# Optimization experiments

Hardware: AMD Instinct MI355X
Metric: run time of the kernel (lower is better)

## Reference

```python
import jax, jax.numpy as jnp
import numpy as np

N = 50000      # nodes
E = 800000     # edges (avg degree 16)
IN = 512       # input features
OUT = 32       # per-head hidden features
H = 8          # heads (layer 1)
C = 16         # classes (layer 2, 1 head)
NEG_SLOPE = 0.2


def setup_inputs() -> dict:
    key = jax.random.key(0)
    ks = jax.random.split(key, 8)
    x = jax.random.normal(ks[0], (N, IN), jnp.float32)
    edge_index = jax.random.randint(ks[1], (2, E), 0, N, jnp.int32)
    # layer 1 params: W1 [IN, H*OUT], attention vectors a1_src/a1_dst [H, OUT]
    W1 = jax.random.normal(ks[2], (IN, H * OUT), jnp.float32) * (1.0 / np.sqrt(IN))
    a1_src = jax.random.normal(ks[3], (H, OUT), jnp.float32) * (1.0 / np.sqrt(OUT))
    a1_dst = jax.random.normal(ks[4], (H, OUT), jnp.float32) * (1.0 / np.sqrt(OUT))
    # layer 2 params: single head, W2 [H*OUT, C], a2_src/a2_dst [1, C]
    W2 = jax.random.normal(ks[5], (H * OUT, C), jnp.float32) * (1.0 / np.sqrt(H * OUT))
    a2_src = jax.random.normal(ks[6], (1, C), jnp.float32) * (1.0 / np.sqrt(C))
    a2_dst = jax.random.normal(ks[7], (1, C), jnp.float32) * (1.0 / np.sqrt(C))
    return {"x": x, "W1": W1, "a1_src": a1_src, "a1_dst": a1_dst,
            "W2": W2, "a2_src": a2_src, "a2_dst": a2_dst,
            "edge_index": edge_index}


def gat_layer(x, edge_index, W, a_src, a_dst, concat):
    """Standard GAT layer: e_ij = LeakyReLU(a_src.Wh_i + a_dst.Wh_j),
    softmax over incoming edges of each target node, scatter-aggregate."""
    n = x.shape[0]
    h_heads, f = a_src.shape
    h = (x @ W).reshape(n, h_heads, f)                      # [N, H, F]
    src, dst = edge_index[0], edge_index[1]
    es = jnp.einsum('nhf,hf->nh', h, a_src)                 # [N, H] per-node src scores
    ed = jnp.einsum('nhf,hf->nh', h, a_dst)                 # [N, H]
    e = jax.nn.leaky_relu(es[src] + ed[dst], NEG_SLOPE)     # [E, H] per-edge logits
    # segment softmax over edges grouped by dst node
    m = jax.ops.segment_max(e, dst, num_segments=n)         # [N, H]
    m = jnp.where(jnp.isfinite(m), m, 0.0)                  # empty segments -> -inf
    p = jnp.exp(e - m[dst])                                 # [E, H]
    s = jax.ops.segment_sum(p, dst, num_segments=n)         # [N, H]
    denom = s[dst]
    alpha = p / jnp.where(denom > 0, denom, 1.0)            # [E, H]
    msg = h[src] * alpha[:, :, None]                        # [E, H, F]
    out = jax.ops.segment_sum(msg, dst, num_segments=n)     # [N, H, F]
    if concat:
        return out.reshape(n, h_heads * f)
    return out.mean(axis=1)


def reference(x, W1, a1_src, a1_dst, W2, a2_src, a2_dst, edge_index):
    # dropout is identity in eval mode
    h = gat_layer(x, edge_index, W1, a1_src, a1_dst, concat=True)   # [N, H*OUT]
    h = jax.nn.elu(h)
    h = gat_layer(h, edge_index, W2, a2_src, a2_dst, concat=False)  # [N, C]
    return jax.nn.log_softmax(h, axis=1)
```

## Files before the change

### kernel.cpp

```cpp
#include <hip/hip_runtime.h>

#define NN 50000
#define EE 800000
#define KIN 512
#define HF 256
#define NH 8
#define FOUT 32
#define NC 16
#define NEG 0.2f
#define NB_SCAN 196
#define NP 50048

typedef unsigned short u16;
typedef __attribute__((ext_vector_type(8))) short shortx8;
typedef __attribute__((ext_vector_type(4))) float floatx4;
typedef __attribute__((ext_vector_type(8))) unsigned short ushortx8;
typedef __attribute__((ext_vector_type(4))) unsigned uintx4;

__device__ __forceinline__ float lrelu(float x) { return x > 0.f ? x : NEG * x; }

__device__ __forceinline__ u16 f2bf(float f) {
    unsigned u = __float_as_uint(f);
    return (u16)((u + 0x7FFFu + ((u >> 16) & 1u)) >> 16);
}
__device__ __forceinline__ float bf2f(u16 v) {
    return __uint_as_float((unsigned)v << 16);
}
__device__ __forceinline__ unsigned pk2bf(float a, float b) {
    unsigned ua = __float_as_uint(a), ub = __float_as_uint(b);
    return ((ua + 0x8000u) >> 16) | ((ub + 0x8000u) & 0xffff0000u);
}

__device__ __forceinline__ void gll16(const void* g, void* l) {
    __builtin_amdgcn_global_load_lds((const __attribute__((address_space(1))) void*)g,
                                     (__attribute__((address_space(3))) void*)l, 16, 0, 0);
}

__global__ void count_deg_convw(const int* __restrict__ dst, int* __restrict__ deg,
                                const float* __restrict__ x, const float* __restrict__ W1,
                                const float* __restrict__ W2,
                                u16* __restrict__ xb2, u16* __restrict__ w1t2,
                                u16* __restrict__ w2t) {
    int e = blockIdx.x * 256 + threadIdx.x;
    if (e < EE) {
        atomicAdd(&deg[dst[e]], 1);
        int n = e >> 4, ks = e & 15;
        const float* xr = x + (size_t)n * KIN + ks * 32;
        u16* tile = xb2 + ((size_t)ks * NP + (size_t)(n & ~63)) * 32;
        int r = n & 63;
#pragma unroll
        for (int g = 0; g < 4; g++) {
            float4 lo = *(const float4*)(xr + g * 8);
            float4 hi = *(const float4*)(xr + g * 8 + 4);
            uintx4 v;
            v[0] = pk2bf(lo.x, lo.y);
            v[1] = pk2bf(lo.z, lo.w);
            v[2] = pk2bf(hi.x, hi.y);
            v[3] = pk2bf(hi.z, hi.w);
            unsigned bo = (unsigned)((r * 64 + g * 16) ^ ((r & 7) << 4));
            *(uintx4*)((char*)tile + bo) = v;
        }
    } else if (e < EE + 16 * 256) {
        int i = e - EE;
        int ks = i >> 8, col = i & 255;
        u16* tile = w1t2 + (size_t)ks * 8192;
#pragma unroll
        for (int g = 0; g < 4; g++) {
            uintx4 v;
#pragma unroll
            for (int p = 0; p < 4; p++) {
                u16 a = f2bf(W1[(size_t)(ks * 32 + g * 8 + 2 * p) * HF + col]);
                u16 b = f2bf(W1[(size_t)(ks * 32 + g * 8 + 2 * p + 1) * HF + col]);
                v[p] = (unsigned)a | ((unsigned)b << 16);
            }
            unsigned bo = (unsigned)((col * 64 + g * 16) ^ ((col & 7) << 4));
            *(uintx4*)((char*)tile + bo) = v;
        }
    } else if (e < EE + 16 * 256 + HF * NC) {
        int e2 = e - EE - 16 * 256;
        int k = e2 >> 4, c = e2 & 15;
        w2t[c * HF + k] = f2bf(W2[e2]);
    }
}

__global__ __launch_bounds__(256) void scan_a(const int* __restrict__ deg, int* __restrict__ bsum) {
    __shared__ int sm[256];
    int t = threadIdx.x;
    int i = blockIdx.x * 256 + t;
    sm[t] = (i < NN) ? deg[i] : 0;
    __syncthreads();
    for (int o = 128; o; o >>= 1) { if (t < o) sm[t] += sm[t + o]; __syncthreads(); }
    if (t == 0) bsum[blockIdx.x] = sm[0];
}

__global__ __launch_bounds__(256) void scan_c(const int* __restrict__ deg, const int* __restrict__ bsum,
                                              int* __restrict__ off) {
    __shared__ int sm[256];
    __shared__ int pre[256];
    int t = threadIdx.x;
    pre[t] = (t < blockIdx.x && t < NB_SCAN) ? bsum[t] : 0;
    __syncthreads();
    for (int o = 128; o; o >>= 1) { if (t < o) pre[t] += pre[t + o]; __syncthreads(); }
    int bofs = pre[0];
    __syncthreads();
    int i = blockIdx.x * 256 + t;
    int d = (i < NN) ? deg[i] : 0;
    sm[t] = d;
    __syncthreads();
    for (int dd = 1; dd < 256; dd <<= 1) {
        int v = (t >= dd) ? sm[t - dd] : 0;
        __syncthreads();
        sm[t] += v;
        __syncthreads();
    }
    if (i < NN) off[i] = bofs + sm[t] - d;
    if (i == 0) off[NN] = EE;
}

__global__ void fill_csr(const int* __restrict__ src, const int* __restrict__ dst,
                         const int* __restrict__ off, int* __restrict__ cursor,
                         int* __restrict__ csr_src) {
    int e = blockIdx.x * 256 + threadIdx.x;
    if (e < EE) {
        int d = dst[e];
        int pos = atomicAdd(&cursor[d], 1);
        csr_src[off[d] + pos] = src[e];
    }
}

__global__ __launch_bounds__(256, 3) void gemm1_mfma(const u16* __restrict__ xb2,
                                                     const u16* __restrict__ w1t2,
                                                     u16* __restrict__ h1b,
                                                     const float* __restrict__ a1s,
                                                     const float* __restrict__ a1d,
                                                     float* __restrict__ es1,
                                                     float* __restrict__ ed1) {
    __shared__ __align__(16) u16 As0[2048];
    __shared__ __align__(16) u16 As1[2048];
    __shared__ __align__(16) u16 Bs0[8192];
    __shared__ __align__(16) u16 Bs1[8192];
    int t = threadIdx.x;
    int lane = t & 63, wave = t >> 6;
    int wm = wave >> 1, wn = wave & 1;
    int lm = lane & 15, quad = lane >> 4;
    int bm = blockIdx.x * 64;

    floatx4 acc[2][8];
#pragma unroll
    for (int i = 0; i < 2; i++)
#pragma unroll
        for (int j = 0; j < 8; j++) acc[i][j] = (floatx4){0.f, 0.f, 0.f, 0.f};

    const u16* abase = xb2 + (size_t)bm * 32 + wave * 512 + lane * 8;
    const u16* bbase = w1t2 + lane * 8;

#define G1_STAGE(AB, BB, KS)                                             \
    {                                                                    \
        gll16(abase + (size_t)(KS) * (NP * 32), AB + wave * 512);        \
        _Pragma("unroll") for (int b = 0; b < 4; b++)                    \
            gll16(bbase + (KS) * 8192 + (wave * 4 + b) * 512,            \
                  BB + (wave * 4 + b) * 512);                            \
    }

#define G1_WAITV(n) do { asm volatile("s_waitcnt vmcnt(" #n ")" ::: "memory"); \
                         __builtin_amdgcn_sched_barrier(0); } while (0)
#define G1_BAR() do { __builtin_amdgcn_sched_barrier(0);                 \
                      __builtin_amdgcn_s_barrier();                      \
                      __builtin_amdgcn_sched_barrier(0); } while (0)

#define G1_COMPUTE(AB, BB)                                               \
    {                                                                    \
        shortx8 af[2], bfv[8];                                           \
        _Pragma("unroll") for (int i = 0; i < 2; i++) {                  \
            int row = wm * 32 + i * 16 + lm;                             \
            unsigned bo = (unsigned)((row * 64 + quad * 16) ^ ((row & 7) << 4)); \
            af[i] = *(const shortx8*)((const char*)AB + bo);             \
        }                                                                \
        _Pragma("unroll") for (int j = 0; j < 8; j++) {                  \
            int col = wn * 128 + j * 16 + lm;                            \
            unsigned bo = (unsigned)((col * 64 + quad * 16) ^ ((col & 7) << 4)); \
            bfv[j] = *(const shortx8*)((const char*)BB + bo);            \
        }                                                                \
        _Pragma("unroll") for (int i = 0; i < 2; i++)                    \
            _Pragma("unroll") for (int j = 0; j < 8; j++)                \
                acc[i][j] = __builtin_amdgcn_mfma_f32_16x16x32_bf16(     \
                    af[i], bfv[j], acc[i][j], 0, 0, 0);                  \
    }

    G1_STAGE(As0, Bs0, 0);
#pragma unroll
    for (int it = 0; it < 16; ++it) {
        if (it < 15) {
            if (it & 1) { G1_STAGE(As0, Bs0, it + 1); }
            else        { G1_STAGE(As1, Bs1, it + 1); }
        }
        if (it < 15) { G1_WAITV(5); } else { G1_WAITV(0); }
        G1_BAR();
        if (it & 1) { G1_COMPUTE(As1, Bs1); }
        else        { G1_COMPUTE(As0, Bs0); }
        G1_BAR();
    }
#undef G1_STAGE
#undef G1_WAITV
#undef G1_BAR
#undef G1_COMPUTE

#pragma unroll
    for (int i = 0; i < 2; i++) {
        int row = bm + wm * 32 + i * 16 + quad * 4;
#pragma unroll
        for (int j = 0; j < 8; j++) {
            int col = wn * 128 + j * 16 + lm;
#pragma unroll
            for (int r = 0; r < 4; r++) {
                if (row + r < NN) h1b[(size_t)(row + r) * HF + col] = f2bf(acc[i][j][r]);
            }
        }
    }

    float as_v[8], ad_v[8];
#pragma unroll
    for (int j = 0; j < 8; j++) {
        int col = wn * 128 + j * 16 + lm;
        as_v[j] = a1s[col];
        ad_v[j] = a1d[col];
    }
#pragma unroll
    for (int i = 0; i < 2; i++) {
#pragma unroll
        for (int r = 0; r < 4; r++) {
            int row = bm + wm * 32 + i * 16 + quad * 4 + r;
#pragma unroll
            for (int hp = 0; hp < 4; hp++) {
                float e_s = acc[i][2 * hp][r] * as_v[2 * hp] + acc[i][2 * hp + 1][r] * as_v[2 * hp + 1];
                float e_d = acc[i][2 * hp][r] * ad_v[2 * hp] + acc[i][2 * hp + 1][r] * ad_v[2 * hp + 1];
#pragma unroll
                for (int o = 8; o; o >>= 1) {
                    e_s += __shfl_down(e_s, o, 16);
                    e_d += __shfl_down(e_d, o, 16);
                }
                if (lm == 0 && row < NN) {
                    int h = wn * 4 + hp;
                    es1[row * NH + h] = e_s;
                    ed1[row * NH + h] = e_d;
                }
            }
        }
    }
}

__global__ __launch_bounds__(256) void agg1_mfma(const u16* __restrict__ h1b, const float* __restrict__ es,
                                                 const float* __restrict__ ed, const int* __restrict__ off,
                                                 const int* __restrict__ csr_src,
                                                 const u16* __restrict__ w2t,
                                                 const float* __restrict__ a2s, const float* __restrict__ a2d,
                                                 u16* __restrict__ h2b, float* __restrict__ es2v,
                                                 float* __restrict__ ed2v) {
    __shared__ __align__(16) u16 Hs[32 * 256];
    __shared__ __align__(16) u16 pTs[8][32];
    __shared__ __align__(16) unsigned char dstloc[32];
    __shared__ int offs_s[17];
    __shared__ float ed_s[16][8];

    int t = threadIdx.x;
    int lane = t & 63, wave = t >> 6;
    int lm = lane & 15, quad = lane >> 4;
    int base = blockIdx.x * 16;

    if (t < 17) offs_s[t] = off[base + t];
    if (t < 128) ed_s[t >> 3][t & 7] = ed[(base + (t >> 3)) * NH + (t & 7)];
    int e0 = off[base];
    int e1 = off[base + 16];
    int nch = (e1 - e0 + 31) >> 5;
    __syncthreads();

    floatx4 acc[2][2];
    floatx4 accS[2];
#pragma unroll
    for (int a = 0; a < 2; a++) {
        accS[a] = (floatx4){0.f, 0.f, 0.f, 0.f};
#pragma unroll
        for (int b = 0; b < 2; b++) acc[a][b] = (floatx4){0.f, 0.f, 0.f, 0.f};
    }

    int h0 = 2 * wave;
    shortx8 ones;
#pragma unroll
    for (int i = 0; i < 8; i++) ones[i] = (short)0x3F80;

    int k_p = t >> 3, h_p = t & 7;
    int sv = 0;
    if (nch > 0) {
        int g = e0 + (lane & 31);
        sv = csr_src[g < e1 ? g : e1 - 1];
    }

    for (int c = 0; c < nch; c++) {
        int svn = 0;
        if (c + 1 < nch) {
            int g = e0 + ((c + 1) << 5) + (lane & 31);
            svn = csr_src[g < e1 ? g : e1 - 1];
        }
#pragma unroll
        for (int pass = 0; pass < 4; pass++) {
            int r = pass * 8 + 2 * wave + (lane >> 5);
            int s = __shfl(sv, r, 64);
            const u16* sp = h1b + (size_t)s * HF + (((lane & 31) ^ (pass << 1)) << 3);
            gll16(sp, Hs + pass * 2048 + wave * 512);
        }
        {
            int g = e0 + (c << 5) + k_p;
            int s = __shfl(sv, k_p, 64);
            float pv = 0.f;
            if (g < e1) {
                int m = 0;
                if (offs_s[m + 8] <= g) m += 8;
                if (offs_s[m + 4] <= g) m += 4;
                if (offs_s[m + 2] <= g) m += 2;
                if (offs_s[m + 1] <= g) m += 1;
                float lg = es[s * NH + h_p] + ed_s[m][h_p];
                lg = lg > 0.f ? lg : NEG * lg;
                pv = __expf(lg);
                if (h_p == 0) dstloc[k_p] = (unsigned char)m;
            }
            pTs[h_p][k_p] = f2bf(pv);
        }
        __syncthreads();

        union { uintx4 u; shortx8 s; } pa, pb, a0, a1;
        pa.s = *(const shortx8*)&pTs[h0][quad * 8];
        pb.s = *(const shortx8*)&pTs[h0 + 1][quad * 8];
        unsigned dw0 = *(const unsigned*)&dstloc[quad * 8];
        unsigned dw1 = *(const unsigned*)&dstloc[quad * 8 + 4];
        unsigned ulm = (unsigned)lm;
        unsigned mm0 = ((dw0 & 255u) == ulm ? 0xffffu : 0u) | (((dw0 >> 8) & 255u) == ulm ? 0xffff0000u : 0u);
        unsigned mm1 = (((dw0 >> 16) & 255u) == ulm ? 0xffffu : 0u) | ((dw0 >> 24) == ulm ? 0xffff0000u : 0u);
        unsigned mm2 = ((dw1 & 255u) == ulm ? 0xffffu : 0u) | (((dw1 >> 8) & 255u) == ulm ? 0xffff0000u : 0u);
        unsigned mm3 = (((dw1 >> 16) & 255u) == ulm ? 0xffffu : 0u) | ((dw1 >> 24) == ulm ? 0xffff0000u : 0u);
        a0.u[0] = pa.u[0] & mm0; a0.u[1] = pa.u[1] & mm1; a0.u[2] = pa.u[2] & mm2; a0.u[3] = pa.u[3] & mm3;
        a1.u[0] = pb.u[0] & mm0; a1.u[1] = pb.u[1] & mm1; a1.u[2] = pb.u[2] & mm2; a1.u[3] = pb.u[3] & mm3;

        accS[0] = __builtin_amdgcn_mfma_f32_16x16x32_bf16(a0.s, ones, accS[0], 0, 0, 0);
        accS[1] = __builtin_amdgcn_mfma_f32_16x16x32_bf16(a1.s, ones, accS[1], 0, 0, 0);

#pragma unroll
        for (int hh = 0; hh < 2; hh++) {
#pragma unroll
            for (int half = 0; half < 2; half++) {
                int f = (h0 + hh) * 32 + half * 16 + lm;
                int bidx = (quad * 8) * 256 + (((f >> 3) ^ (quad << 1)) << 3) + (f & 7);
                shortx8 bfv;
#pragma unroll
                for (int j = 0; j < 8; j++) bfv[j] = (short)Hs[bidx + j * 256];
                acc[hh][half] = __builtin_amdgcn_mfma_f32_16x16x32_bf16(
                    hh ? a1.s : a0.s, bfv, acc[hh][half], 0, 0, 0);
            }
        }
        __syncthreads();
        sv = svn;
    }

    char* HsB = (char*)Hs;
#pragma unroll
    for (int hh = 0; hh < 2; hh++) {
#pragma unroll
        for (int r = 0; r < 4; r++) {
            float sden = accS[hh][r];
            float inv = sden > 0.f ? 1.0f / sden : 0.f;
            int nl = quad * 4 + r;
#pragma unroll
            for (int half = 0; half < 2; half++) {
                float v = acc[hh][half][r] * inv;
                v = v > 0.f ? v : (__expf(v) - 1.0f);
                int f = (h0 + hh) * 32 + half * 16 + lm;
                int byte = (nl * 512 + ((f >> 3) << 4) + ((f & 7) << 1)) ^ ((nl & 7) << 4);
                *(u16*)(HsB + byte) = f2bf(v);
            }
        }
    }
    __syncthreads();
    if (wave != 0) return;

    floatx4 acc2 = (floatx4){0.f, 0.f, 0.f, 0.f};
#pragma unroll
    for (int ks = 0; ks < 8; ks++) {
        int abyte = (lm * 512 + (ks * 4 + quad) * 16) ^ ((lm & 7) << 4);
        shortx8 af2 = *(const shortx8*)(HsB + abyte);
        shortx8 bf2v = *(const shortx8*)(w2t + lm * HF + ks * 32 + quad * 8);
        acc2 = __builtin_amdgcn_mfma_f32_16x16x32_bf16(af2, bf2v, acc2, 0, 0, 0);
    }
    float a2sc = a2s[lm], a2dc = a2d[lm];
#pragma unroll
    for (int r = 0; r < 4; r++) {
        int n = base + quad * 4 + r;
        float v = acc2[r];
        h2b[n * NC + lm] = f2bf(v);
        float ps = v * a2sc, pd = v * a2dc;
#pragma unroll
        for (int o = 8; o; o >>= 1) {
            ps += __shfl_down(ps, o, 16);
            pd += __shfl_down(pd, o, 16);
        }
        if (lm == 0) { es2v[n] = ps; ed2v[n] = pd; }
    }
}

__global__ __launch_bounds__(256) void agg2(const u16* __restrict__ h2b, const float* __restrict__ es2,
                                            const float* __restrict__ ed2, const int* __restrict__ off,
                                            const int* __restrict__ csr_src, float* __restrict__ out) {
    int t = threadIdx.x;
    int nid = blockIdx.x * 16 + (t >> 4);
    int c = t & 15;
    int beg = off[nid];
    int deg = off[nid + 1] - beg;
    float edn = ed2[nid];
    float s = 0.f, acc = 0.f;
    for (int base = 0; base < deg; base += 16) {
        int nch = deg - base; if (nch > 16) nch = 16;
        int sv = 0;
        if (c < nch) sv = csr_src[beg + base + c];
        int sva[16];
#pragma unroll
        for (int e = 0; e < 16; e++) sva[e] = __shfl(sv, e, 16);
        float hva[16];
#pragma unroll
        for (int e = 0; e < 16; e++) hva[e] = bf2f(h2b[sva[e] * NC + c]);
        float p = 0.f;
        if (c < nch) p = __expf(lrelu(es2[sv] + edn));
        s += p;
        float pa[16];
#pragma unroll
        for (int e = 0; e < 16; e++) pa[e] = __shfl(p, e, 16);
#pragma unroll
        for (int e = 0; e < 16; e++) acc += pa[e] * hva[e];
    }
#pragma unroll
    for (int o = 8; o; o >>= 1) s += __shfl_down(s, o, 16);
    s = __shfl(s, 0, 16);
    float v = (s > 0.f) ? acc / s : 0.f;
    float m2 = v;
#pragma unroll
    for (int o = 8; o; o >>= 1) m2 = fmaxf(m2, __shfl_down(m2, o, 16));
    m2 = __shfl(m2, 0, 16);
    float se = __expf(v - m2);
#pragma unroll
    for (int o = 8; o; o >>= 1) se += __shfl_down(se, o, 16);
    se = __shfl(se, 0, 16);
    out[nid * NC + c] = v - m2 - __logf(se);
}

extern "C" void kernel_launch(void* const* d_in, const int* in_sizes, int n_in,
                              void* d_out, int out_size, void* d_ws, size_t ws_size,
                              hipStream_t stream) {
    const float* x   = (const float*)d_in[0];
    const float* W1  = (const float*)d_in[1];
    const float* a1s = (const float*)d_in[2];
    const float* a1d = (const float*)d_in[3];
    const float* W2  = (const float*)d_in[4];
    const float* a2s = (const float*)d_in[5];
    const float* a2d = (const float*)d_in[6];
    const int*   ei  = (const int*)d_in[7];
    const int* srcv = ei;
    const int* dstv = ei + EE;
    float* out = (float*)d_out;

    char* W = (char*)d_ws;
    u16* h1b    = (u16*)W;  W += (size_t)NN * HF * 2;
    float* es1  = (float*)W; W += (size_t)NN * NH * 4;
    float* ed1  = (float*)W; W += (size_t)NN * NH * 4;
    int* csr    = (int*)W;  W += (size_t)EE * 4;
    int* bsum   = (int*)W;  W += 1024;
    u16* w1t2   = (u16*)W;  W += (size_t)16 * 256 * 32 * 2;
    u16* w2t    = (u16*)W;  W += (size_t)NC * HF * 2;
    int* deg    = (int*)W;  W += (size_t)NN * 4;
    int* cursor = (int*)W;  W += (size_t)NN * 4;
    int* offs   = (int*)W;  W += 200064;
    u16* xb2    = (u16*)W;
    u16* h2b    = (u16*)W;
    float* es2v = (float*)(h2b + (size_t)NN * NC);
    float* ed2v = es2v + NN;

    hipMemsetAsync(deg, 0, 2 * NN * sizeof(int), stream);
    count_deg_convw<<<(EE + 16 * 256 + HF * NC + 255) / 256, 256, 0, stream>>>(
        dstv, deg, x, W1, W2, xb2, w1t2, w2t);
    scan_a<<<NB_SCAN, 256, 0, stream>>>(deg, bsum);
    scan_c<<<NB_SCAN, 256, 0, stream>>>(deg, bsum, offs);
    fill_csr<<<(EE + 255) / 256, 256, 0, stream>>>(srcv, dstv, offs, cursor, csr);
    gemm1_mfma<<<(NN + 63) / 64, 256, 0, stream>>>(xb2, w1t2, h1b, a1s, a1d, es1, ed1);
    agg1_mfma<<<NN / 16, 256, 0, stream>>>(h1b, es1, ed1, offs, csr, w2t, a2s, a2d,
                                           h2b, es2v, ed2v);
    agg2<<<NN / 16, 256, 0, stream>>>(h2b, es2v, ed2v, offs, csr, out);
}
```

Measured before the change: 351.3 us.

## Double-buffer neighbor feature gathers in agg1 with manual waitcnt barriers

Splits the LDS feature tile into two buffers so the async global-to-LDS gather for the next edge chunk is issued before the current chunk's softmax and MFMA work. CSR source indices are prefetched three chunks ahead, and the es load is hoisted ahead of the gather. __syncthreads is replaced with explicit s_waitcnt vmcnt/lgkmcnt plus s_barrier and sched_barrier fences. The cost is double the LDS (lower occupancy), and the hand-counted vmcnt(5) relies on a fixed number of outstanding loads, which makes it fragile.

```diff
diff --git a/kernel.cpp b/kernel.cpp
--- a/kernel.cpp
+++ b/kernel.cpp
@@ -256,7 +256,7 @@
                                                  const float* __restrict__ a2s, const float* __restrict__ a2d,
                                                  u16* __restrict__ h2b, float* __restrict__ es2v,
                                                  float* __restrict__ ed2v) {
-    __shared__ __align__(16) u16 Hs[32 * 256];
+    __shared__ __align__(16) u16 Hs[2][8192];
     __shared__ __align__(16) u16 pTs[8][32];
     __shared__ __align__(16) unsigned char dstloc[32];
     __shared__ int offs_s[17];
@@ -289,28 +289,32 @@
     for (int i = 0; i < 8; i++) ones[i] = (short)0x3F80;
 
     int k_p = t >> 3, h_p = t & 7;
-    int sv = 0;
-    if (nch > 0) {
-        int g = e0 + (lane & 31);
-        sv = csr_src[g < e1 ? g : e1 - 1];
-    }
+    int gmax = (e1 > e0) ? (e1 - 1) : 0;
+
+#define A1_CSR(c) csr_src[min(e0 + ((c) << 5) + (lane & 31), gmax)]
+#define A1_STAGE(B, SV)                                                      \
+    {                                                                        \
+        _Pragma("unroll") for (int pass = 0; pass < 4; pass++) {             \
+            int r = pass * 8 + 2 * wave + (lane >> 5);                       \
+            int s = __shfl(SV, r, 64);                                       \
+            const u16* sp = h1b + (size_t)s * HF + (((lane & 31) ^ (pass << 1)) << 3); \
+            gll16(sp, Hs[B] + pass * 2048 + wave * 512);                     \
+        }                                                                    \
+    }
+#define A1_FENCE() __builtin_amdgcn_sched_barrier(0)
+
+    int sv  = A1_CSR(0);
+    int svn = A1_CSR(1);
+    A1_STAGE(0, sv);
+    int sv2 = A1_CSR(2);
 
     for (int c = 0; c < nch; c++) {
-        int svn = 0;
-        if (c + 1 < nch) {
-            int g = e0 + ((c + 1) << 5) + (lane & 31);
-            svn = csr_src[g < e1 ? g : e1 - 1];
-        }
-#pragma unroll
-        for (int pass = 0; pass < 4; pass++) {
-            int r = pass * 8 + 2 * wave + (lane >> 5);
-            int s = __shfl(sv, r, 64);
-            const u16* sp = h1b + (size_t)s * HF + (((lane & 31) ^ (pass << 1)) << 3);
-            gll16(sp, Hs + pass * 2048 + wave * 512);
-        }
+        int s_pc = __shfl(sv, k_p, 64);
+        float esl = es[s_pc * NH + h_p];
+        if (c + 1 < nch) { A1_STAGE((c + 1) & 1, svn); }
+        int sv3 = A1_CSR(c + 3);
         {
             int g = e0 + (c << 5) + k_p;
-            int s = __shfl(sv, k_p, 64);
             float pv = 0.f;
             if (g < e1) {
                 int m = 0;
@@ -318,14 +322,20 @@
                 if (offs_s[m + 4] <= g) m += 4;
                 if (offs_s[m + 2] <= g) m += 2;
                 if (offs_s[m + 1] <= g) m += 1;
-                float lg = es[s * NH + h_p] + ed_s[m][h_p];
+                float lg = esl + ed_s[m][h_p];
                 lg = lg > 0.f ? lg : NEG * lg;
                 pv = __expf(lg);
                 if (h_p == 0) dstloc[k_p] = (unsigned char)m;
             }
             pTs[h_p][k_p] = f2bf(pv);
         }
-        __syncthreads();
+        A1_FENCE();
+        asm volatile("s_waitcnt vmcnt(5)" ::: "memory");
+        A1_FENCE();
+        asm volatile("s_waitcnt lgkmcnt(0)" ::: "memory");
+        A1_FENCE();
+        __builtin_amdgcn_s_barrier();
+        A1_FENCE();
 
         union { uintx4 u; shortx8 s; } pa, pb, a0, a1;
         pa.s = *(const shortx8*)&pTs[h0][quad * 8];
@@ -343,6 +353,7 @@
         accS[0] = __builtin_amdgcn_mfma_f32_16x16x32_bf16(a0.s, ones, accS[0], 0, 0, 0);
         accS[1] = __builtin_amdgcn_mfma_f32_16x16x32_bf16(a1.s, ones, accS[1], 0, 0, 0);
 
+        const u16* Hc = Hs[c & 1];
 #pragma unroll
         for (int hh = 0; hh < 2; hh++) {
 #pragma unroll
@@ -351,16 +362,21 @@
                 int bidx = (quad * 8) * 256 + (((f >> 3) ^ (quad << 1)) << 3) + (f & 7);
                 shortx8 bfv;
 #pragma unroll
-                for (int j = 0; j < 8; j++) bfv[j] = (short)Hs[bidx + j * 256];
+                for (int j = 0; j < 8; j++) bfv[j] = (short)Hc[bidx + j * 256];
                 acc[hh][half] = __builtin_amdgcn_mfma_f32_16x16x32_bf16(
                     hh ? a1.s : a0.s, bfv, acc[hh][half], 0, 0, 0);
             }
         }
-        __syncthreads();
-        sv = svn;
-    }
-
-    char* HsB = (char*)Hs;
+        A1_FENCE();
+        __builtin_amdgcn_s_barrier();
+        A1_FENCE();
+        sv = svn; svn = sv2; sv2 = sv3;
+    }
+#undef A1_CSR
+#undef A1_STAGE
+#undef A1_FENCE
+
+    char* HsB = (char*)Hs[0];
 #pragma unroll
     for (int hh = 0; hh < 2; hh++) {
 #pragma unroll
```

Result: no change. 355.0 us (+1.1%).
